# Kernel tuning notes

Hardware: AMD Instinct MI355X
Metric: run time of the kernel (lower is better)

The kernel has to match this reference:

```python
import jax, jax.numpy as jnp
import numpy as np

B, N, D, H = 4, 1024, 768, 12
DH = D // H
HIDDEN = 4 * D
EPS = 1e-6


def _layernorm(x, g, b):
    mu = jnp.mean(x, axis=-1, keepdims=True)
    var = jnp.mean(jnp.square(x - mu), axis=-1, keepdims=True)
    return (x - mu) * jax.lax.rsqrt(var + EPS) * g + b


def setup_inputs() -> dict:
    key = jax.random.key(0)
    ks = jax.random.split(key, 8)
    s = 0.02  # init scale for weights
    return {
        "x": jax.random.normal(ks[0], (B, N, D), jnp.float32),
        "adj_bias": jax.random.normal(ks[1], (N, N), jnp.float32) * 0.1,
        "ln1_g": jnp.ones((D,), jnp.float32),
        "ln1_b": jnp.zeros((D,), jnp.float32),
        "qkv_w": jax.random.normal(ks[2], (D, 3 * D), jnp.float32) * s,
        "qkv_b": jnp.zeros((3 * D,), jnp.float32),
        "proj_w": jax.random.normal(ks[3], (D, D), jnp.float32) * s,
        "proj_b": jnp.zeros((D,), jnp.float32),
        "ln2_g": jnp.ones((D,), jnp.float32),
        "ln2_b": jnp.zeros((D,), jnp.float32),
        "fc1_w": jax.random.normal(ks[4], (D, HIDDEN), jnp.float32) * s,
        "fc1_b": jnp.zeros((HIDDEN,), jnp.float32),
        "fc2_w": jax.random.normal(ks[5], (HIDDEN, D), jnp.float32) * s,
        "fc2_b": jnp.zeros((D,), jnp.float32),
    }


def reference(x, adj_bias, ln1_g, ln1_b, qkv_w, qkv_b, proj_w, proj_b,
              ln2_g, ln2_b, fc1_w, fc1_b, fc2_w, fc2_b):
    scale = DH ** -0.5
    # --- attention with additive adjacency bias ---
    h = _layernorm(x, ln1_g, ln1_b)
    qkv = (h @ qkv_w + qkv_b).reshape(B, N, 3, H, DH)
    q, k, v = (jnp.moveaxis(qkv, 2, 0)[i].transpose(0, 2, 1, 3) for i in range(3))  # [B,H,N,DH]
    scores = jnp.einsum('bhqd,bhkd->bhqk', q, k) * scale + adj_bias[None, None]
    w = jax.nn.softmax(scores, axis=-1)
    attn = jnp.einsum('bhqk,bhkd->bhqd', w, v)          # [B,H,N,DH]
    attn = attn.transpose(0, 2, 1, 3).reshape(B, N, D)  # [B,N,D]
    x = x + (attn @ proj_w + proj_b)
    # --- MLP ---
    h2 = _layernorm(x, ln2_g, ln2_b)
    m = jax.nn.gelu(h2 @ fc1_w + fc1_b, approximate=False) @ fc2_w + fc2_b
    return x + m
```

## Files before the change

### kernel.cpp

```cpp
#include <hip/hip_runtime.h>
#include <cstdint>
#include <cstring>

typedef unsigned short u16;
typedef __attribute__((ext_vector_type(8))) short short8;
typedef __attribute__((ext_vector_type(4))) float float4v;

#define BB 4
#define NN 1024
#define DD 768
#define HH 12
#define DHH 64
#define HID 3072
#define MM (BB*NN)

__device__ __forceinline__ u16 f2b(float f) {
  unsigned int u = __float_as_uint(f);
  u += 0x7FFF + ((u >> 16) & 1);
  return (u16)(u >> 16);
}
__device__ __forceinline__ float b2f(u16 h) {
  return __uint_as_float(((unsigned int)h) << 16);
}

__device__ __forceinline__ void gll16(const void* g, void* l) {
  __builtin_amdgcn_global_load_lds(
      (const __attribute__((address_space(1))) unsigned int*)g,
      (__attribute__((address_space(3))) unsigned int*)l, 16, 0, 0);
}

__global__ __launch_bounds__(256)
void prep_k(const float* __restrict__ qkvw, const float* __restrict__ projw,
            const float* __restrict__ fc1w, const float* __restrict__ fc2w,
            const float* __restrict__ adj,
            u16* __restrict__ wtqkv, u16* __restrict__ wtproj,
            u16* __restrict__ wtfc1, u16* __restrict__ wtfc2,
            u16* __restrict__ adjP) {
  __shared__ float tile[32][33];
  const int id = blockIdx.x, t = threadIdx.x;
  if (id < 6912) {
    const float* w; u16* wt; int K, N, tid;
    if (id < 1728)      { w = qkvw;  wt = wtqkv;  K = DD;  N = 3 * DD; tid = id; }
    else if (id < 2304) { w = projw; wt = wtproj; K = DD;  N = DD;     tid = id - 1728; }
    else if (id < 4608) { w = fc1w;  wt = wtfc1;  K = DD;  N = HID;    tid = id - 2304; }
    else                { w = fc2w;  wt = wtfc2;  K = HID; N = DD;     tid = id - 4608; }
    const int ntiles = N / 32;
    const int n0 = (tid % ntiles) * 32, k0 = (tid / ntiles) * 32;
    const int tx = t & 31, ty = t >> 5;
#pragma unroll
    for (int i = 0; i < 4; i++)
      tile[ty + i * 8][tx] = w[(size_t)(k0 + ty + i * 8) * N + n0 + tx];
    __syncthreads();
#pragma unroll
    for (int i = 0; i < 4; i++)
      wt[(size_t)(n0 + ty + i * 8) * K + k0 + tx] = f2b(tile[tx][ty + i * 8]);
  } else {
    const int aid = id - 6912;
    const int qt = aid >> 4, kt = aid & 15;
    const int wv = t >> 6, q4 = (t >> 4) & 3, m15 = t & 15;
    u16 v[16];
#pragma unroll
    for (int ct = 0; ct < 4; ct++)
#pragma unroll
      for (int r = 0; r < 4; r++)
        v[ct * 4 + r] =
            f2b(adj[(size_t)(qt * 64 + wv * 16 + q4 * 4 + r) * NN + kt * 64 + ct * 16 + m15]);
    u16* dst = adjP + (size_t)aid * 4096 + t * 16;
    *(uint4*)dst = *(const uint4*)&v[0];
    *(uint4*)(dst + 8) = *(const uint4*)&v[8];
  }
}

__global__ __launch_bounds__(256)
void ln_k(const float* __restrict__ x, const float* __restrict__ g,
          const float* __restrict__ b, u16* __restrict__ o) {
  const int row = blockIdx.x, t = threadIdx.x;
  const float* xr = x + (size_t)row * DD;
  float v0 = xr[t], v1 = xr[t + 256], v2 = xr[t + 512];
  float s = v0 + v1 + v2;
  float s2 = v0 * v0 + v1 * v1 + v2 * v2;
#pragma unroll
  for (int off = 32; off > 0; off >>= 1) {
    s += __shfl_down(s, off);
    s2 += __shfl_down(s2, off);
  }
  __shared__ float rs[4], rs2[4], bc[2];
  const int lane = t & 63, wv = t >> 6;
  if (lane == 0) { rs[wv] = s; rs2[wv] = s2; }
  __syncthreads();
  if (t == 0) {
    float ts = rs[0] + rs[1] + rs[2] + rs[3];
    float ts2 = rs2[0] + rs2[1] + rs2[2] + rs2[3];
    float mean = ts * (1.f / DD);
    float var = ts2 * (1.f / DD) - mean * mean;
    bc[0] = mean;
    bc[1] = rsqrtf(var + 1e-6f);
  }
  __syncthreads();
  const float mean = bc[0], rstd = bc[1];
  u16* orow = o + (size_t)row * DD;
  orow[t]       = f2b((v0 - mean) * rstd * g[t]       + b[t]);
  orow[t + 256] = f2b((v1 - mean) * rstd * g[t + 256] + b[t + 256]);
  orow[t + 512] = f2b((v2 - mean) * rstd * g[t + 512] + b[t + 512]);
}

template <int MODE, int TN, int NC>
__global__ __launch_bounds__(256, 4)
void gemm_k(const u16* __restrict__ A, const u16* __restrict__ Bt,
            const float* __restrict__ bias, const float* __restrict__ resid,
            float* __restrict__ outf, u16* __restrict__ outb,
            u16* __restrict__ outq, u16* __restrict__ outk, u16* __restrict__ outv,
            int K) {
  constexpr int DP = (TN == 64) ? 4 : 3;
  __shared__ u16 As[DP][128 * 32];
  __shared__ u16 Bs[DP][TN * 32];
  constexpr int JM = TN / 32;
  constexpr int VC = (TN == 128) ? 4 : 3;
  constexpr int NB = NC / TN;
  constexpr int RN = NB / 2;

  const int id = blockIdx.x;
  const int xcd = id & 7, idx = id >> 3;
  const int tileN = ((xcd & 1) * RN + idx % RN) * TN;
  const int tileM = ((xcd >> 1) * 8 + idx / RN) * 128;

  const int lane = threadIdx.x & 63, wave = threadIdx.x >> 6;
  const int wrow = (wave >> 1) * 64, wcol = (wave & 1) * (TN / 2);
  const int m15 = lane & 15, q4 = lane >> 4;
  const int sw = (q4 ^ ((m15 >> 1) & 3)) * 8;

  float4v acc[4][JM];
#pragma unroll
  for (int i = 0; i < 4; i++)
#pragma unroll
    for (int j = 0; j < JM; j++) acc[i][j] = (float4v)0.f;

  auto stage = [&](int kt, int buf) {
    const int kk0 = kt * 32;
#pragma unroll
    for (int q = wave; q < 8; q += 4) {
      const int c = q * 64 + lane;
      gll16(A + (size_t)(tileM + (c >> 2)) * K + kk0 + ((c & 3) ^ ((c >> 3) & 3)) * 8,
            &As[buf][q * 512]);
    }
#pragma unroll
    for (int q = wave; q < TN / 16; q += 4) {
      const int c = q * 64 + lane;
      gll16(Bt + (size_t)(tileN + (c >> 2)) * K + kk0 + ((c & 3) ^ ((c >> 3) & 3)) * 8,
            &Bs[buf][q * 512]);
    }
  };

  auto compute = [&](int buf) {
    short8 af[4], bfr[JM];
#pragma unroll
    for (int i = 0; i < 4; i++)
      af[i] = *(const short8*)(&As[buf][(wrow + i * 16 + m15) * 32 + sw]);
#pragma unroll
    for (int j = 0; j < JM; j++)
      bfr[j] = *(const short8*)(&Bs[buf][(wcol + j * 16 + m15) * 32 + sw]);
#pragma unroll
    for (int i = 0; i < 4; i++)
#pragma unroll
      for (int j = 0; j < JM; j++)
        acc[i][j] = __builtin_amdgcn_mfma_f32_16x16x32_bf16(af[i], bfr[j], acc[i][j], 0, 0, 0);
  };

  const int T = K >> 5;
#pragma unroll
  for (int d = 0; d < DP; d++) stage(d, d);

  int cur = 0;
  for (int kt = 0; kt < T - DP; ++kt) {
    asm volatile("s_waitcnt vmcnt(%0)\n\ts_barrier" :: "n"((DP - 1) * VC) : "memory");
    compute(cur);
    asm volatile("s_waitcnt lgkmcnt(0)\n\ts_barrier" ::: "memory");
    stage(kt + DP, cur);
    cur = (cur == DP - 1) ? 0 : cur + 1;
  }
  if constexpr (DP == 4) {
    asm volatile("s_waitcnt vmcnt(%0)\n\ts_barrier" :: "n"(3 * VC) : "memory");
    compute(cur);
    asm volatile("s_waitcnt lgkmcnt(0)\n\ts_barrier" ::: "memory");
    cur = (cur == DP - 1) ? 0 : cur + 1;
  }
  asm volatile("s_waitcnt vmcnt(%0)\n\ts_barrier" :: "n"(2 * VC) : "memory");
  compute(cur);
  asm volatile("s_waitcnt lgkmcnt(0)\n\ts_barrier" ::: "memory");
  cur = (cur == DP - 1) ? 0 : cur + 1;
  asm volatile("s_waitcnt vmcnt(%0)\n\ts_barrier" :: "n"(VC) : "memory");
  compute(cur);
  asm volatile("s_waitcnt lgkmcnt(0)\n\ts_barrier" ::: "memory");
  cur = (cur == DP - 1) ? 0 : cur + 1;
  asm volatile("s_waitcnt vmcnt(0)\n\ts_barrier" ::: "memory");
  compute(cur);

#pragma unroll
  for (int i = 0; i < 4; i++) {
#pragma unroll
    for (int j = 0; j < JM; j++) {
      const int col = tileN + wcol + j * 16 + m15;
#pragma unroll
      for (int r = 0; r < 4; r++) {
        const int row = tileM + wrow + i * 16 + q4 * 4 + r;
        float v = acc[i][j][r] + bias[col];
        if (MODE == 1) {
          outf[(size_t)row * NC + col] = resid[(size_t)row * NC + col] + v;
        } else if (MODE == 2) {
          float gv = 0.5f * v * (1.f + erff(v * 0.70710678f));
          outb[(size_t)row * NC + col] = f2b(gv);
        } else {
          const int three = col / DD, hh = (col % DD) >> 6, dh = col & 63;
          const int bb = row >> 10, nn = row & 1023;
          if (three == 2) {
            outv[(((size_t)(bb * HH + hh)) * DHH + dh) * NN + nn] = f2b(v);
          } else {
            const size_t idx2 = (((size_t)(bb * HH + hh)) * NN + nn) * DHH + dh;
            (three == 0 ? outq : outk)[idx2] = f2b(v);
          }
        }
      }
    }
  }
}

__global__ __launch_bounds__(256, 4)
void attn_k(const u16* __restrict__ qw, const u16* __restrict__ kw,
            const u16* __restrict__ vtw, const u16* __restrict__ adjP,
            u16* __restrict__ out) {
  __shared__ u16 Ks[64][72];
  __shared__ u16 Vt[64][72];
  __shared__ u16 Pb[4][16][72];

  const int id = blockIdx.x;
  const int bh = (id & 7) * 6 + ((id >> 3) >> 4);
  const int qt = (id >> 3) & 15;
  const int t = threadIdx.x, lane = t & 63, wave = t >> 6;
  const int m15 = lane & 15, q4 = lane >> 4;

  const u16* qrow = qw + ((size_t)bh * NN + qt * 64 + wave * 16 + m15) * DHH;
  const short8 qf0 = *(const short8*)(qrow + q4 * 8);
  const short8 qf1 = *(const short8*)(qrow + 32 + q4 * 8);

  float lreg[4] = {0.f, 0.f, 0.f, 0.f};
  float4v o[4];
#pragma unroll
  for (int ct = 0; ct < 4; ct++) o[ct] = (float4v)0.f;

  const u16* kbase0 = kw + (size_t)bh * NN * DHH;
  const u16* vtbase0 = vtw + (size_t)bh * DHH * NN;
  const u16* abase = adjP + (size_t)qt * 16 * 4096 + t * 16;

  const int r0 = t >> 3;
  const int c80 = (t & 7) * 8;

  uint4 kr0 = *(const uint4*)(kbase0 + r0 * 64 + c80);
  uint4 kr1 = *(const uint4*)(kbase0 + (r0 + 32) * 64 + c80);
  uint4 vr0 = *(const uint4*)(vtbase0 + (size_t)r0 * NN + c80);
  uint4 vr1 = *(const uint4*)(vtbase0 + (size_t)(r0 + 32) * NN + c80);

  for (int kt = 0; kt < 16; kt++) {
    __syncthreads();
    *(uint4*)&Ks[r0][c80] = kr0;
    *(uint4*)&Ks[r0 + 32][c80] = kr1;
    *(uint4*)&Vt[r0][c80] = vr0;
    *(uint4*)&Vt[r0 + 32][c80] = vr1;
    __syncthreads();
    if (kt < 15) {
      const u16* kb = kbase0 + (size_t)(kt + 1) * 64 * DHH;
      const u16* vb = vtbase0 + (kt + 1) * 64;
      kr0 = *(const uint4*)(kb + r0 * 64 + c80);
      kr1 = *(const uint4*)(kb + (r0 + 32) * 64 + c80);
      vr0 = *(const uint4*)(vb + (size_t)r0 * NN + c80);
      vr1 = *(const uint4*)(vb + (size_t)(r0 + 32) * NN + c80);
    }
    u16 av[16];
    const u16* ap = abase + (size_t)kt * 4096;
    *(uint4*)&av[0] = *(const uint4*)ap;
    *(uint4*)&av[8] = *(const uint4*)(ap + 8);

    float4v s[4];
#pragma unroll
    for (int ct = 0; ct < 4; ct++) s[ct] = (float4v)0.f;
#pragma unroll
    for (int ct = 0; ct < 4; ct++) {
      short8 b = *(const short8*)&Ks[ct * 16 + m15][q4 * 8];
      s[ct] = __builtin_amdgcn_mfma_f32_16x16x32_bf16(qf0, b, s[ct], 0, 0, 0);
    }
#pragma unroll
    for (int ct = 0; ct < 4; ct++) {
      short8 b = *(const short8*)&Ks[ct * 16 + m15][32 + q4 * 8];
      s[ct] = __builtin_amdgcn_mfma_f32_16x16x32_bf16(qf1, b, s[ct], 0, 0, 0);
    }

#pragma unroll
    for (int ct = 0; ct < 4; ct++)
#pragma unroll
      for (int r = 0; r < 4; r++) {
        float v = s[ct][r] * 0.125f + b2f(av[ct * 4 + r]);
        u16 pb = f2b(__expf(v));
        Pb[wave][q4 * 4 + r][ct * 16 + m15] = pb;
        lreg[r] += b2f(pb);
      }

    asm volatile("s_waitcnt lgkmcnt(0)" ::: "memory");

    short8 a0 = *(const short8*)&Pb[wave][m15][q4 * 8];
    short8 a1 = *(const short8*)&Pb[wave][m15][32 + q4 * 8];
#pragma unroll
    for (int ct = 0; ct < 4; ct++) {
      short8 b = *(const short8*)&Vt[ct * 16 + m15][q4 * 8];
      o[ct] = __builtin_amdgcn_mfma_f32_16x16x32_bf16(a0, b, o[ct], 0, 0, 0);
    }
#pragma unroll
    for (int ct = 0; ct < 4; ct++) {
      short8 b = *(const short8*)&Vt[ct * 16 + m15][32 + q4 * 8];
      o[ct] = __builtin_amdgcn_mfma_f32_16x16x32_bf16(a1, b, o[ct], 0, 0, 0);
    }
  }

#pragma unroll
  for (int off = 1; off < 16; off <<= 1)
#pragma unroll
    for (int r = 0; r < 4; r++) lreg[r] += __shfl_xor(lreg[r], off);

  const int bb2 = bh / HH, hh = bh % HH;
  const int row0 = qt * 64 + wave * 16 + q4 * 4;
#pragma unroll
  for (int ct = 0; ct < 4; ct++)
#pragma unroll
    for (int r = 0; r < 4; r++)
      out[((size_t)(bb2 * NN + row0 + r)) * DD + hh * 64 + ct * 16 + m15] =
          f2b(o[ct][r] / lreg[r]);
}

extern "C" void kernel_launch(void* const* d_in, const int* in_sizes, int n_in,
                              void* d_out, int out_size, void* d_ws, size_t ws_size,
                              hipStream_t stream) {
  const float* x     = (const float*)d_in[0];
  const float* adj   = (const float*)d_in[1];
  const float* ln1g  = (const float*)d_in[2];
  const float* ln1b  = (const float*)d_in[3];
  const float* qkvw  = (const float*)d_in[4];
  const float* qkvb  = (const float*)d_in[5];
  const float* projw = (const float*)d_in[6];
  const float* projb = (const float*)d_in[7];
  const float* ln2g  = (const float*)d_in[8];
  const float* ln2b  = (const float*)d_in[9];
  const float* fc1w  = (const float*)d_in[10];
  const float* fc1b  = (const float*)d_in[11];
  const float* fc2w  = (const float*)d_in[12];
  const float* fc2b  = (const float*)d_in[13];
  float* out = (float*)d_out;

  char* ws = (char*)d_ws;
  u16* wtqkv = (u16*)ws;  ws += (size_t)DD * (3 * DD) * 2;
  u16* wtproj = (u16*)ws; ws += (size_t)DD * DD * 2;
  u16* wtfc1 = (u16*)ws;  ws += (size_t)DD * HID * 2;
  u16* wtfc2 = (u16*)ws;  ws += (size_t)HID * DD * 2;
  u16* adjP = (u16*)ws;   ws += (size_t)NN * NN * 2;
  u16* hbuf = (u16*)ws;   ws += (size_t)MM * DD * 2;
  u16* qws = (u16*)ws;    ws += (size_t)MM * DD * 2;
  u16* kws = (u16*)ws;    ws += (size_t)MM * DD * 2;
  u16* vtws = (u16*)ws;   ws += (size_t)MM * DD * 2;
  u16* attnb = (u16*)ws;  ws += (size_t)MM * DD * 2;
  u16* h2buf = (u16*)ws;  ws += (size_t)MM * DD * 2;
  u16* a1buf = (u16*)ws;  ws += (size_t)MM * HID * 2;

  prep_k<<<7168, 256, 0, stream>>>(qkvw, projw, fc1w, fc2w, adj,
                                   wtqkv, wtproj, wtfc1, wtfc2, adjP);

  ln_k<<<MM, 256, 0, stream>>>(x, ln1g, ln1b, hbuf);

  gemm_k<0, 128, 3 * DD><<<((3 * DD) / 128) * (MM / 128), 256, 0, stream>>>(
      hbuf, wtqkv, qkvb, nullptr, nullptr, nullptr, qws, kws, vtws, DD);

  attn_k<<<(NN / 64) * (BB * HH), 256, 0, stream>>>(qws, kws, vtws, adjP, attnb);

  gemm_k<1, 64, DD><<<(DD / 64) * (MM / 128), 256, 0, stream>>>(
      attnb, wtproj, projb, x, out, nullptr, nullptr, nullptr, nullptr, DD);

  ln_k<<<MM, 256, 0, stream>>>(out, ln2g, ln2b, h2buf);

  gemm_k<2, 128, HID><<<(HID / 128) * (MM / 128), 256, 0, stream>>>(
      h2buf, wtfc1, fc1b, nullptr, nullptr, a1buf, nullptr, nullptr, nullptr, DD);

  gemm_k<1, 64, DD><<<(DD / 64) * (MM / 128), 256, 0, stream>>>(
      a1buf, wtfc2, fc2b, out, out, nullptr, nullptr, nullptr, nullptr, HID);
}
```

Before: 305.3 us.

## Switch GEMM to double-buffered pipeline with configurable K tile depth

Replaces the 3/4-deep multi-stage LDS prefetch pipeline in the GEMM kernel with a simple double buffer, and adds a BK template parameter so the proj and fc2 GEMMs use a 64-wide K tile with an 8-way XOR swizzle. Issuing the next stage before computing is meant to keep loads in flight while halving the barrier count per K for the BK=64 cases. The shallower prefetch depth may expose more global-load latency, especially for the BK=32 QKV and fc1 GEMMs.

```diff
diff --git a/kernel.cpp b/kernel.cpp
--- a/kernel.cpp
+++ b/kernel.cpp
@@ -104,18 +104,21 @@
   orow[t + 512] = f2b((v2 - mean) * rstd * g[t + 512] + b[t + 512]);
 }
 
-template <int MODE, int TN, int NC>
+template <int MODE, int TN, int BK, int NC>
 __global__ __launch_bounds__(256, 4)
 void gemm_k(const u16* __restrict__ A, const u16* __restrict__ Bt,
             const float* __restrict__ bias, const float* __restrict__ resid,
             float* __restrict__ outf, u16* __restrict__ outb,
             u16* __restrict__ outq, u16* __restrict__ outk, u16* __restrict__ outv,
             int K) {
-  constexpr int DP = (TN == 64) ? 4 : 3;
-  __shared__ u16 As[DP][128 * 32];
-  __shared__ u16 Bs[DP][TN * 32];
+  __shared__ u16 As[2][128 * BK];
+  __shared__ u16 Bs[2][TN * BK];
   constexpr int JM = TN / 32;
-  constexpr int VC = (TN == 128) ? 4 : 3;
+  constexpr int KK = BK / 32;
+  constexpr int SLOTS = BK / 8;
+  constexpr int AI = BK / 4;
+  constexpr int BI = TN * BK / 512;
+  constexpr int VC = (AI + BI) / 4;
   constexpr int NB = NC / TN;
   constexpr int RN = NB / 2;
 
@@ -127,7 +130,7 @@
   const int lane = threadIdx.x & 63, wave = threadIdx.x >> 6;
   const int wrow = (wave >> 1) * 64, wcol = (wave & 1) * (TN / 2);
   const int m15 = lane & 15, q4 = lane >> 4;
-  const int sw = (q4 ^ ((m15 >> 1) & 3)) * 8;
+  const int rkey = (BK == 32) ? ((m15 >> 1) & 3) : (m15 & 7);
 
   float4v acc[4][JM];
 #pragma unroll
@@ -136,64 +139,56 @@
     for (int j = 0; j < JM; j++) acc[i][j] = (float4v)0.f;
 
   auto stage = [&](int kt, int buf) {
-    const int kk0 = kt * 32;
-#pragma unroll
-    for (int q = wave; q < 8; q += 4) {
+    const int kk0 = kt * BK;
+#pragma unroll
+    for (int q = wave; q < AI; q += 4) {
       const int c = q * 64 + lane;
-      gll16(A + (size_t)(tileM + (c >> 2)) * K + kk0 + ((c & 3) ^ ((c >> 3) & 3)) * 8,
-            &As[buf][q * 512]);
-    }
-#pragma unroll
-    for (int q = wave; q < TN / 16; q += 4) {
+      const int row = c / SLOTS, slot = c % SLOTS;
+      const int key = (BK == 32) ? ((row >> 1) & 3) : (row & 7);
+      gll16(A + (size_t)(tileM + row) * K + kk0 + (slot ^ key) * 8, &As[buf][q * 512]);
+    }
+#pragma unroll
+    for (int q = wave; q < BI; q += 4) {
       const int c = q * 64 + lane;
-      gll16(Bt + (size_t)(tileN + (c >> 2)) * K + kk0 + ((c & 3) ^ ((c >> 3) & 3)) * 8,
-            &Bs[buf][q * 512]);
+      const int row = c / SLOTS, slot = c % SLOTS;
+      const int key = (BK == 32) ? ((row >> 1) & 3) : (row & 7);
+      gll16(Bt + (size_t)(tileN + row) * K + kk0 + (slot ^ key) * 8, &Bs[buf][q * 512]);
     }
   };
 
-  auto compute = [&](int buf) {
-    short8 af[4], bfr[JM];
+  const int T = K / BK;
+  stage(0, 0);
+  for (int kt = 0; kt < T; ++kt) {
+    const int cur = kt & 1;
+    if (kt + 1 < T) {
+      stage(kt + 1, cur ^ 1);
+      asm volatile("s_waitcnt vmcnt(%0)\n\ts_barrier" :: "n"(VC) : "memory");
+    } else {
+      asm volatile("s_waitcnt vmcnt(0)\n\ts_barrier" ::: "memory");
+    }
+    short8 af[4][KK], bfr[JM][KK];
 #pragma unroll
     for (int i = 0; i < 4; i++)
-      af[i] = *(const short8*)(&As[buf][(wrow + i * 16 + m15) * 32 + sw]);
+#pragma unroll
+      for (int kk = 0; kk < KK; kk++)
+        af[i][kk] = *(const short8*)(
+            &As[cur][(wrow + i * 16 + m15) * BK + (((kk * 4 + q4) ^ rkey)) * 8]);
 #pragma unroll
     for (int j = 0; j < JM; j++)
-      bfr[j] = *(const short8*)(&Bs[buf][(wcol + j * 16 + m15) * 32 + sw]);
+#pragma unroll
+      for (int kk = 0; kk < KK; kk++)
+        bfr[j][kk] = *(const short8*)(
+            &Bs[cur][(wcol + j * 16 + m15) * BK + (((kk * 4 + q4) ^ rkey)) * 8]);
 #pragma unroll
     for (int i = 0; i < 4; i++)
 #pragma unroll
       for (int j = 0; j < JM; j++)
-        acc[i][j] = __builtin_amdgcn_mfma_f32_16x16x32_bf16(af[i], bfr[j], acc[i][j], 0, 0, 0);
-  };
-
-  const int T = K >> 5;
-#pragma unroll
-  for (int d = 0; d < DP; d++) stage(d, d);
-
-  int cur = 0;
-  for (int kt = 0; kt < T - DP; ++kt) {
-    asm volatile("s_waitcnt vmcnt(%0)\n\ts_barrier" :: "n"((DP - 1) * VC) : "memory");
-    compute(cur);
+#pragma unroll
+        for (int kk = 0; kk < KK; kk++)
+          acc[i][j] =
+              __builtin_amdgcn_mfma_f32_16x16x32_bf16(af[i][kk], bfr[j][kk], acc[i][j], 0, 0, 0);
     asm volatile("s_waitcnt lgkmcnt(0)\n\ts_barrier" ::: "memory");
-    stage(kt + DP, cur);
-    cur = (cur == DP - 1) ? 0 : cur + 1;
-  }
-  if constexpr (DP == 4) {
-    asm volatile("s_waitcnt vmcnt(%0)\n\ts_barrier" :: "n"(3 * VC) : "memory");
-    compute(cur);
-    asm volatile("s_waitcnt lgkmcnt(0)\n\ts_barrier" ::: "memory");
-    cur = (cur == DP - 1) ? 0 : cur + 1;
-  }
-  asm volatile("s_waitcnt vmcnt(%0)\n\ts_barrier" :: "n"(2 * VC) : "memory");
-  compute(cur);
-  asm volatile("s_waitcnt lgkmcnt(0)\n\ts_barrier" ::: "memory");
-  cur = (cur == DP - 1) ? 0 : cur + 1;
-  asm volatile("s_waitcnt vmcnt(%0)\n\ts_barrier" :: "n"(VC) : "memory");
-  compute(cur);
-  asm volatile("s_waitcnt lgkmcnt(0)\n\ts_barrier" ::: "memory");
-  cur = (cur == DP - 1) ? 0 : cur + 1;
-  asm volatile("s_waitcnt vmcnt(0)\n\ts_barrier" ::: "memory");
-  compute(cur);
+  }
 
 #pragma unroll
   for (int i = 0; i < 4; i++) {
@@ -372,19 +367,19 @@
 
   ln_k<<<MM, 256, 0, stream>>>(x, ln1g, ln1b, hbuf);
 
-  gemm_k<0, 128, 3 * DD><<<((3 * DD) / 128) * (MM / 128), 256, 0, stream>>>(
+  gemm_k<0, 128, 32, 3 * DD><<<((3 * DD) / 128) * (MM / 128), 256, 0, stream>>>(
       hbuf, wtqkv, qkvb, nullptr, nullptr, nullptr, qws, kws, vtws, DD);
 
   attn_k<<<(NN / 64) * (BB * HH), 256, 0, stream>>>(qws, kws, vtws, adjP, attnb);
 
-  gemm_k<1, 64, DD><<<(DD / 64) * (MM / 128), 256, 0, stream>>>(
+  gemm_k<1, 64, 64, DD><<<(DD / 64) * (MM / 128), 256, 0, stream>>>(
       attnb, wtproj, projb, x, out, nullptr, nullptr, nullptr, nullptr, DD);
 
   ln_k<<<MM, 256, 0, stream>>>(out, ln2g, ln2b, h2buf);
 
-  gemm_k<2, 128, HID><<<(HID / 128) * (MM / 128), 256, 0, stream>>>(
+  gemm_k<2, 128, 32, HID><<<(HID / 128) * (MM / 128), 256, 0, stream>>>(
       h2buf, wtfc1, fc1b, nullptr, nullptr, a1buf, nullptr, nullptr, nullptr, DD);
 
-  gemm_k<1, 64, DD><<<(DD / 64) * (MM / 128), 256, 0, stream>>>(
+  gemm_k<1, 64, 64, DD><<<(DD / 64) * (MM / 128), 256, 0, stream>>>(
       a1buf, wtfc2, fc2b, out, out, nullptr, nullptr, nullptr, nullptr, HID);
 }
```

Measured after the change: 284.9 us. 1.07x faster.
